# Kernel tuning notes

Hardware: AMD Instinct MI355X
Metric: run time of the kernel (lower is better)

The kernel has to match this reference:

```python
import jax, jax.numpy as jnp
import numpy as np

B, T, I, H, L = 64, 1024, 256, 512, 2

def setup_inputs() -> dict:
    key = jax.random.key(0)
    ks = jax.random.split(key, 1 + 4 * L)
    inp = {"x": jax.random.normal(ks[0], (B, 1, I, T), dtype=jnp.float32)}
    s_in = 1.0 / np.sqrt(H)
    for l in range(L):
        in_dim = I if l == 0 else H
        k0, k1, k2, k3 = ks[1 + 4 * l: 5 + 4 * l]
        inp[f"W_ih{l}"] = jax.random.uniform(k0, (4 * H, in_dim), jnp.float32, -s_in, s_in)
        inp[f"W_hh{l}"] = jax.random.uniform(k1, (4 * H, H), jnp.float32, -s_in, s_in)
        inp[f"b_ih{l}"] = jax.random.uniform(k2, (4 * H,), jnp.float32, -s_in, s_in)
        inp[f"b_hh{l}"] = jax.random.uniform(k3, (4 * H,), jnp.float32, -s_in, s_in)
    return inp

def _lstm_layer(x, W_ih, W_hh, b_ih, b_hh):
    # x: [B, T, in_dim] -> outputs [B, T, H], (h_T, c_T) each [B, H]
    xp = jnp.einsum('bti,gi->btg', x, W_ih) + b_ih + b_hh  # [B, T, 4H]
    h0 = jnp.zeros((x.shape[0], H), x.dtype)
    c0 = jnp.zeros((x.shape[0], H), x.dtype)

    def step(carry, xt):
        h, c = carry
        gates = xt + h @ W_hh.T  # [B, 4H]
        i, f, g, o = jnp.split(gates, 4, axis=-1)  # PyTorch gate order: i,f,g,o
        i = jax.nn.sigmoid(i); f = jax.nn.sigmoid(f)
        g = jnp.tanh(g); o = jax.nn.sigmoid(o)
        c = f * c + i * g
        h = o * jnp.tanh(c)
        return (h, c), h

    (hT, cT), ys = jax.lax.scan(step, (h0, c0), jnp.swapaxes(xp, 0, 1))
    return jnp.swapaxes(ys, 0, 1), hT, cT

def reference(x, W_ih0, W_hh0, b_ih0, b_hh0, W_ih1, W_hh1, b_ih1, b_hh1):
    # x: [B, 1, I, T] -> squeeze(1), permute(0,2,1) -> [B, T, I]
    seq = jnp.transpose(jnp.squeeze(x, 1), (0, 2, 1))
    params = [(W_ih0, W_hh0, b_ih0, b_hh0), (W_ih1, W_hh1, b_ih1, b_hh1)]
    hs, cs = [], []
    out = seq
    for (W_ih, W_hh, b_ih, b_hh) in params:
        out, hT, cT = _lstm_layer(out, W_ih, W_hh, b_ih, b_hh)
        hs.append(hT); cs.append(cT)
    hidden = jnp.stack(hs, 0)  # [L, B, H]
    cell = jnp.stack(cs, 0)    # [L, B, H]
    return (out, (hidden, cell))
```

## Files before the change

kernel.cpp:

```cpp
#include <hip/hip_runtime.h>

#define HB 64
#define HT 1024
#define HI 256
#define HH 512

typedef short short8 __attribute__((ext_vector_type(8)));
typedef float f32x4 __attribute__((ext_vector_type(4)));
typedef int   i32x4 __attribute__((ext_vector_type(4)));

__device__ __forceinline__ unsigned short f2bf(float f) {
    unsigned u = __float_as_uint(f);
    u += 0x7FFF + ((u >> 16) & 1);
    return (unsigned short)(u >> 16);
}
__device__ __forceinline__ float bf2f(unsigned short s) {
    return __uint_as_float(((unsigned)s) << 16);
}
__device__ __forceinline__ float fsigmoid(float x) {
    return __builtin_amdgcn_rcpf(1.0f + __expf(-x));
}
__device__ __forceinline__ float ftanh(float x) {
    return 1.0f - 2.0f * __builtin_amdgcn_rcpf(__expf(2.0f * x) + 1.0f);
}

__device__ __forceinline__ void st_pair16(void* p, i32x4 v) {
    asm volatile("global_store_dwordx4 %0, %1, off sc0 sc1"
                 :: "v"(p), "v"(v) : "memory");
}

__device__ __forceinline__ void lds_fence() {
    asm volatile("s_waitcnt lgkmcnt(0)" ::: "memory");
    __builtin_amdgcn_sched_barrier(0);
}

__device__ __forceinline__ void pull16(const char* base0, int expect, short8* af,
                                       int& fuel) {
    for (;;) {
        i32x4 v[32];
        const char* b = base0;
        #pragma unroll
        for (int bi = 0; bi < 8; ++bi) {
            asm volatile("global_load_dwordx4 %0, %1, off sc0 sc1"
                         : "=v"(v[bi * 4 + 0]) : "v"(b));
            asm volatile("global_load_dwordx4 %0, %1, off offset:16 sc0 sc1"
                         : "=v"(v[bi * 4 + 1]) : "v"(b));
            asm volatile("global_load_dwordx4 %0, %1, off offset:2048 sc0 sc1"
                         : "=v"(v[bi * 4 + 2]) : "v"(b));
            asm volatile("global_load_dwordx4 %0, %1, off offset:2064 sc0 sc1"
                         : "=v"(v[bi * 4 + 3]) : "v"(b));
            b += 4096;
        }
        asm volatile("s_waitcnt vmcnt(0)" ::: "memory");
        __builtin_amdgcn_sched_barrier(0);
        int ok = 1;
        #pragma unroll
        for (int i = 0; i < 32; ++i)
            ok &= (v[i][2] == expect) & (v[i][3] == 0);
        bool done = (__ballot(ok != 0) == ~0ull);
        if (!done) {
            fuel -= 64;
            if (fuel > 0) { __builtin_amdgcn_s_sleep(2); continue; }
        }
        #pragma unroll
        for (int kt = 0; kt < 16; ++kt) {
            union { int i4[4]; short8 s; } u;
            u.i4[0] = v[2 * kt][0];     u.i4[1] = v[2 * kt][1];
            u.i4[2] = v[2 * kt + 1][0]; u.i4[3] = v[2 * kt + 1][1];
            af[kt] = u.s;
        }
        return;
    }
}

__global__ void pack_weights(const float* __restrict__ Wih0, const float* __restrict__ Whh0,
                             const float* __restrict__ bih0, const float* __restrict__ bhh0,
                             const float* __restrict__ Wih1, const float* __restrict__ Whh1,
                             const float* __restrict__ bih1, const float* __restrict__ bhh1,
                             unsigned short* __restrict__ wp0,
                             unsigned short* __restrict__ wp1,
                             float* __restrict__ bs) {
    int idx = blockIdx.x * 256 + threadIdx.x;
    int stride = gridDim.x * 256;
    const int NP0 = 128 * 24 * 512;
    const int NP1 = 128 * 32 * 512;
    for (int e = idx; e < NP0; e += stride) {
        int j = e & 7, l = (e >> 3) & 63, rem = e >> 9;
        int kt = rem % 24, nt = rem / 24;
        int n = nt * 16 + (l & 15);
        int k = kt * 32 + ((l >> 4) << 3) + j;
        float v = (k < HI) ? Wih0[n * HI + k] : Whh0[n * HH + (k - HI)];
        wp0[e] = f2bf(v);
    }
    for (int e = idx; e < NP1; e += stride) {
        int j = e & 7, l = (e >> 3) & 63, rem = e >> 9;
        int kt = rem & 31, nt = rem >> 5;
        int n = nt * 16 + (l & 15);
        int k = kt * 32 + ((l >> 4) << 3) + j;
        float v = (k < HH) ? Wih1[n * HH + k] : Whh1[n * HH + (k - HH)];
        wp1[e] = f2bf(v);
    }
    for (int e = idx; e < 2048; e += stride) {
        bs[e]        = bih0[e] + bhh0[e];
        bs[2048 + e] = bih1[e] + bhh1[e];
    }
}

__global__ void pack_x(const float* __restrict__ x, unsigned short* __restrict__ xp) {
    int tt = blockIdx.x;
    int ii = blockIdx.y;
    int bt = blockIdx.z;
    int w  = threadIdx.x;
    __shared__ unsigned short tile[512][16];
    int tloc = w & 15;
    for (int q = 0; q < 32; ++q) {
        int p = q * 16 + (w >> 4);
        int m = p >> 5, iloc = p & 31;
        int b = bt * 16 + m, i = ii * 32 + iloc, t = tt * 16 + tloc;
        tile[p][tloc] = f2bf(x[((size_t)b * HI + i) * HT + t]);
    }
    __syncthreads();
    int e  = w * 2;
    int l  = e >> 3, j0 = e & 7;
    int m  = l & 15;
    int i0 = ((l >> 4) << 3) + j0;
    for (int ti = 0; ti < 16; ++ti) {
        int t = tt * 16 + ti;
        size_t base = ((size_t)(t * 4 + bt) * 8 + ii) * 512;
        unsigned v0 = tile[m * 32 + i0][ti];
        unsigned v1 = tile[m * 32 + i0 + 1][ti];
        ((unsigned int*)xp)[(base + e) >> 1] = v0 | (v1 << 16);
    }
}

__global__ void init_sync(int* __restrict__ flags,
                          int4* __restrict__ h0r, int4* __restrict__ h1r) {
    int idx = blockIdx.x * 256 + threadIdx.x;
    int stride = gridDim.x * 256;
    for (int e = idx; e < 256; e += stride) flags[e] = 0;
    int4 s; s.x = 0; s.y = 0; s.z = -1; s.w = -1;
    for (int e = idx; e < 32768; e += stride) h0r[e] = s;
    for (int e = idx; e < 16384; e += stride) h1r[e] = s;
}

__global__ void __launch_bounds__(256, 1) lstm_persist(
        const unsigned short* __restrict__ wp0,
        const unsigned short* __restrict__ wp1,
        const float* __restrict__ bs,
        const unsigned short* __restrict__ xp,
        char* __restrict__ h0ring,
        char* __restrict__ h1ring,
        int* __restrict__ flag0,
        int* __restrict__ flag1,
        float* __restrict__ out) {
    __shared__ int4 ldsw[8192];
    __shared__ unsigned short stage_s[1024];

    const int bid   = blockIdx.x;
    const int layer = bid >> 5;
    const int ut    = bid & 31;
    const int tid   = threadIdx.x;
    const int mt    = tid >> 6;
    const int l     = tid & 63;
    const int ul    = l & 15;
    const int q     = l >> 4;
    const int KT    = layer ? 32 : 24;

    const short8* ldsf = (const short8*)ldsw;

    {
        const unsigned short* wsrc = layer ? wp1 : wp0;
        for (int g = 0; g < 4; ++g) {
            const int4* src = (const int4*)(wsrc + (size_t)(g * 32 + ut) * KT * 512);
            int4* dst = ldsw + (size_t)g * KT * 64;
            for (int i = tid; i < KT * 64; i += 256) dst[i] = src[i];
        }
    }
    float bv[4];
    #pragma unroll
    for (int g = 0; g < 4; ++g) bv[g] = bs[layer * 2048 + g * HH + ut * 16 + ul];
    float cc[4] = {0.f, 0.f, 0.f, 0.f};
    __syncthreads();

    const int u = ut * 16 + ul;
    const int stg_w = mt * 256 + (ul >> 3) * 128 + (ul & 7);
    const int ring_sub = (ut >> 1) * 128 + ((2 * ut) & 3) * 32 + l;

    const int* pp0 = (l < 32) ? (flag0 + mt * 32 + l)
                              : (flag1 + mt * 32 + (l - 32));
    const int* pp1 = flag1 + mt * 32 + (l & 31);

    int fuel = 1 << 23;

    for (int t = 0; t < HT; ++t) {
        f32x4 acc[4];
        #pragma unroll
        for (int g = 0; g < 4; ++g) {
            f32x4 a; a[0] = bv[g]; a[1] = bv[g]; a[2] = bv[g]; a[3] = bv[g];
            acc[g] = a;
        }

        if (layer == 0) {
            const bool act  = (l < 32) ? (t > 0) : (t >= 4);
            const int  need = (l < 32) ? t : (t - 3);
            int pf = act ? __hip_atomic_load(pp0, __ATOMIC_RELAXED,
                                             __HIP_MEMORY_SCOPE_AGENT)
                         : 0x7fffffff;

            const short8* xa = (const short8*)xp + ((size_t)t * 4 + mt) * 8 * 64;
            #pragma unroll
            for (int kt = 0; kt < 8; ++kt) {
                short8 a = xa[kt * 64 + l];
                #pragma unroll
                for (int g = 0; g < 4; ++g)
                    acc[g] = __builtin_amdgcn_mfma_f32_16x16x32_bf16(
                        a, ldsf[(g * 24 + kt) * 64 + l], acc[g], 0, 0, 0);
            }
            if (t > 0) {
                for (;;) {
                    if (__ballot(pf >= need) == ~0ull) break;
                    if (--fuel <= 0) break;
                    __builtin_amdgcn_s_sleep(1);
                    if (act) pf = __hip_atomic_load(pp0, __ATOMIC_RELAXED,
                                                    __HIP_MEMORY_SCOPE_AGENT);
                }
                const char* hb = h0ring +
                    (size_t)((((t - 1) & 3) * 4 + mt)) * 32768 + (size_t)l * 32;
                short8 af[16];
                pull16(hb, t - 1, af, fuel);
                #pragma unroll
                for (int kt = 0; kt < 16; ++kt) {
                    #pragma unroll
                    for (int g = 0; g < 4; ++g)
                        acc[g] = __builtin_amdgcn_mfma_f32_16x16x32_bf16(
                            af[kt], ldsf[(g * 24 + 8 + kt) * 64 + l], acc[g], 0, 0, 0);
                }
            }

            #pragma unroll
            for (int r = 0; r < 4; ++r) {
                int m = q * 4 + r;
                int b = mt * 16 + m;
                float iv = fsigmoid(acc[0][r]);
                float fv2 = fsigmoid(acc[1][r]);
                float gv = ftanh(acc[2][r]);
                float ov = fsigmoid(acc[3][r]);
                float c = fv2 * cc[r] + iv * gv;
                cc[r] = c;
                float h = ov * ftanh(c);
                stage_s[stg_w + m * 8] = f2bf(h);
                if (t == HT - 1) {
                    out[33554432 + b * 512 + u] = h;
                    out[33619968 + b * 512 + u] = c;
                }
            }
            lds_fence();

            {
                unsigned s0 = stage_s[tid * 4 + 0], s1 = stage_s[tid * 4 + 1];
                unsigned s2 = stage_s[tid * 4 + 2], s3 = stage_s[tid * 4 + 3];
                i32x4 pv;
                pv[0] = (int)(s0 | (s1 << 16));
                pv[1] = (int)(s2 | (s3 << 16));
                pv[2] = t; pv[3] = 0;
                char* dst = h0ring +
                    ((size_t)((t & 3) * 4 + mt) * 2048 + ring_sub) * 16;
                st_pair16(dst, pv);
            }
            if (l == 0)
                __hip_atomic_store(flag0 + mt * 32 + ut, t + 1,
                                   __ATOMIC_RELAXED, __HIP_MEMORY_SCOPE_AGENT);
            asm volatile("s_waitcnt vmcnt(0)" ::: "memory");
        } else {
            int pf = (t > 0 && l < 32)
                         ? __hip_atomic_load(pp1, __ATOMIC_RELAXED,
                                             __HIP_MEMORY_SCOPE_AGENT)
                         : 0x7fffffff;

            if (t > 0) {
                for (;;) {
                    if (__ballot(pf >= t) == ~0ull) break;
                    if (--fuel <= 0) break;
                    __builtin_amdgcn_s_sleep(1);
                    if (l < 32) pf = __hip_atomic_load(pp1, __ATOMIC_RELAXED,
                                                       __HIP_MEMORY_SCOPE_AGENT);
                }
                const char* hb1 = h1ring +
                    (size_t)((((t - 1) & 1) * 4 + mt)) * 32768 + (size_t)l * 32;
                short8 af1[16];
                pull16(hb1, t - 1, af1, fuel);
                #pragma unroll
                for (int kt = 0; kt < 16; ++kt) {
                    #pragma unroll
                    for (int g = 0; g < 4; ++g)
                        acc[g] = __builtin_amdgcn_mfma_f32_16x16x32_bf16(
                            af1[kt], ldsf[(g * 32 + 16 + kt) * 64 + l], acc[g], 0, 0, 0);
                }
            }
            {
                const char* hb0 = h0ring +
                    (size_t)(((t & 3) * 4 + mt)) * 32768 + (size_t)l * 32;
                short8 af0[16];
                pull16(hb0, t, af0, fuel);
                #pragma unroll
                for (int kt = 0; kt < 16; ++kt) {
                    #pragma unroll
                    for (int g = 0; g < 4; ++g)
                        acc[g] = __builtin_amdgcn_mfma_f32_16x16x32_bf16(
                            af0[kt], ldsf[(g * 32 + kt) * 64 + l], acc[g], 0, 0, 0);
                }
            }

            #pragma unroll
            for (int r = 0; r < 4; ++r) {
                int m = q * 4 + r;
                int b = mt * 16 + m;
                float iv = fsigmoid(acc[0][r]);
                float fv2 = fsigmoid(acc[1][r]);
                float gv = ftanh(acc[2][r]);
                float ov = fsigmoid(acc[3][r]);
                float c = fv2 * cc[r] + iv * gv;
                cc[r] = c;
                float h = ov * ftanh(c);
                stage_s[stg_w + m * 8] = f2bf(h);
                if (t == HT - 1) {
                    out[33554432 + 32768 + b * 512 + u] = h;
                    out[33619968 + 32768 + b * 512 + u] = c;
                }
            }
            lds_fence();

            {
                unsigned s0 = stage_s[tid * 4 + 0], s1 = stage_s[tid * 4 + 1];
                unsigned s2 = stage_s[tid * 4 + 2], s3 = stage_s[tid * 4 + 3];
                i32x4 pv;
                pv[0] = (int)(s0 | (s1 << 16));
                pv[1] = (int)(s2 | (s3 << 16));
                pv[2] = t; pv[3] = 0;
                char* dst = h1ring +
                    ((size_t)((t & 1) * 4 + mt) * 2048 + ring_sub) * 16;
                st_pair16(dst, pv);
            }
            if (l == 0)
                __hip_atomic_store(flag1 + mt * 32 + ut, t + 1,
                                   __ATOMIC_RELAXED, __HIP_MEMORY_SCOPE_AGENT);

            {
                int lb = l >> 2, ch = l & 3;
                int b = mt * 16 + lb;
                const unsigned short* sp = stage_s + mt * 256 + (ch >> 1) * 128 +
                                           lb * 8 + (ch & 1) * 4;
                f32x4 o;
                o[0] = bf2f(sp[0]); o[1] = bf2f(sp[1]);
                o[2] = bf2f(sp[2]); o[3] = bf2f(sp[3]);
                *(f32x4*)&out[((size_t)b * HT + t) * HH + ut * 16 + ch * 4] = o;
            }
            asm volatile("s_waitcnt vmcnt(0)" ::: "memory");
        }
    }
}

extern "C" void kernel_launch(void* const* d_in, const int* in_sizes, int n_in,
                              void* d_out, int out_size, void* d_ws, size_t ws_size,
                              hipStream_t stream) {
    const float* x    = (const float*)d_in[0];
    const float* Wih0 = (const float*)d_in[1];
    const float* Whh0 = (const float*)d_in[2];
    const float* bih0 = (const float*)d_in[3];
    const float* bhh0 = (const float*)d_in[4];
    const float* Wih1 = (const float*)d_in[5];
    const float* Whh1 = (const float*)d_in[6];
    const float* bih1 = (const float*)d_in[7];
    const float* bhh1 = (const float*)d_in[8];

    char* ws = (char*)d_ws;
    unsigned short* wp0 = (unsigned short*)(ws + 0);
    unsigned short* wp1 = (unsigned short*)(ws + 3145728);
    float*          bsv = (float*)(ws + 7340032);
    unsigned short* xp  = (unsigned short*)(ws + 7356416);
    int*   flag0        = (int*)(ws + 40910848);
    int*   flag1        = (int*)(ws + 40911360);
    char*  h0r          = (char*)(ws + 41041920);
    char*  h1r          = (char*)(ws + 41566208);
    float* out = (float*)d_out;

    pack_weights<<<2048, 256, 0, stream>>>(Wih0, Whh0, bih0, bhh0,
                                           Wih1, Whh1, bih1, bhh1, wp0, wp1, bsv);
    pack_x<<<dim3(64, 8, 4), 256, 0, stream>>>(x, xp);
    init_sync<<<64, 256, 0, stream>>>(flag0, (int4*)h0r, (int4*)h1r);

    lstm_persist<<<64, 256, 0, stream>>>(wp0, wp1, bsv, xp, h0r, h1r,
                                         flag0, flag1, out);
}
```

Baseline: 7.487 ms.

## Pin each LSTM layer to one XCD and sync via local L2 instead of MALL

The kernel now launches 256 blocks and uses the XCC_ID register with atomic slot counters so that layer 0 runs on XCD 0 and layer 1 on XCD 1, and surplus blocks exit. Intra-layer hidden-state exchange uses sc0-only stores and loads plus buffer_inv, keeping the polling traffic in the XCD-local L2 rather than going to MALL. Only the layer0-to-layer1 handoff still goes through a MALL ring. Ring buffers are no longer reinitialised on each launch: a generation counter (rb) is bumped every call and embedded in the tags, and explicit flag polling is replaced by tag checks. This relies on the hardware dispatching at least 32 blocks to each of XCDs 0 and 1, and on sc0 coherence semantics holding within one XCD.

```diff
diff --git a/kernel.cpp b/kernel.cpp
--- a/kernel.cpp
+++ b/kernel.cpp
@@ -24,18 +24,65 @@
     return 1.0f - 2.0f * __builtin_amdgcn_rcpf(__expf(2.0f * x) + 1.0f);
 }
 
-__device__ __forceinline__ void st_pair16(void* p, i32x4 v) {
-    asm volatile("global_store_dwordx4 %0, %1, off sc0 sc1"
-                 :: "v"(p), "v"(v) : "memory");
-}
-
+__device__ __forceinline__ void st_pair_loc(void* p, i32x4 v) {
+    asm volatile("global_store_dwordx4 %0, %1, off sc0" :: "v"(p), "v"(v) : "memory");
+}
+__device__ __forceinline__ void st_pair_mall(void* p, i32x4 v) {
+    asm volatile("global_store_dwordx4 %0, %1, off sc0 sc1" :: "v"(p), "v"(v) : "memory");
+}
 __device__ __forceinline__ void lds_fence() {
     asm volatile("s_waitcnt lgkmcnt(0)" ::: "memory");
     __builtin_amdgcn_sched_barrier(0);
 }
-
-__device__ __forceinline__ void pull16(const char* base0, int expect, short8* af,
-                                       int& fuel) {
+__device__ __forceinline__ int ld4m(const int* p) {
+    int v;
+    asm volatile("global_load_dword %0, %1, off sc0 sc1" : "=v"(v) : "v"(p) : "memory");
+    asm volatile("s_waitcnt vmcnt(0)" ::: "memory");
+    __builtin_amdgcn_sched_barrier(0);
+    return v;
+}
+
+__device__ __forceinline__ void pull16_loc(const char* base0, int expect,
+                                           short8* af, int& fuel) {
+    for (;;) {
+        asm volatile("buffer_inv" ::: "memory");
+        i32x4 v[32];
+        const char* b = base0;
+        #pragma unroll
+        for (int bi = 0; bi < 8; ++bi) {
+            asm volatile("global_load_dwordx4 %0, %1, off sc0"
+                         : "=v"(v[bi * 4 + 0]) : "v"(b));
+            asm volatile("global_load_dwordx4 %0, %1, off offset:16 sc0"
+                         : "=v"(v[bi * 4 + 1]) : "v"(b));
+            asm volatile("global_load_dwordx4 %0, %1, off offset:2048 sc0"
+                         : "=v"(v[bi * 4 + 2]) : "v"(b));
+            asm volatile("global_load_dwordx4 %0, %1, off offset:2064 sc0"
+                         : "=v"(v[bi * 4 + 3]) : "v"(b));
+            b += 4096;
+        }
+        asm volatile("s_waitcnt vmcnt(0)" ::: "memory");
+        __builtin_amdgcn_sched_barrier(0);
+        int ok = 1;
+        #pragma unroll
+        for (int i = 0; i < 32; ++i)
+            ok &= (v[i][2] == expect) & (v[i][3] == 0);
+        bool done = (__ballot(ok != 0) == ~0ull);
+        if (!done) {
+            fuel -= 64;
+            if (fuel > 0) { __builtin_amdgcn_s_sleep(2); continue; }
+        }
+        #pragma unroll
+        for (int kt = 0; kt < 16; ++kt) {
+            union { int i4[4]; short8 s; } u;
+            u.i4[0] = v[2 * kt][0];     u.i4[1] = v[2 * kt][1];
+            u.i4[2] = v[2 * kt + 1][0]; u.i4[3] = v[2 * kt + 1][1];
+            af[kt] = u.s;
+        }
+        return;
+    }
+}
+__device__ __forceinline__ void pull16_mall(const char* base0, int expect,
+                                            short8* af, int& fuel) {
     for (;;) {
         i32x4 v[32];
         const char* b = base0;
@@ -133,14 +180,10 @@
     }
 }
 
-__global__ void init_sync(int* __restrict__ flags,
-                          int4* __restrict__ h0r, int4* __restrict__ h1r) {
-    int idx = blockIdx.x * 256 + threadIdx.x;
-    int stride = gridDim.x * 256;
-    for (int e = idx; e < 256; e += stride) flags[e] = 0;
-    int4 s; s.x = 0; s.y = 0; s.z = -1; s.w = -1;
-    for (int e = idx; e < 32768; e += stride) h0r[e] = s;
-    for (int e = idx; e < 16384; e += stride) h1r[e] = s;
+__global__ void init_sync(int* __restrict__ s) {
+    int i = threadIdx.x;
+    if (i == 0) { s[0] = 0; s[1] = 0; s[2] += 2048; }
+    if (i >= 64 && i < 192) s[i] = 0;
 }
 
 __global__ void __launch_bounds__(256, 1) lstm_persist(
@@ -148,24 +191,43 @@
         const unsigned short* __restrict__ wp1,
         const float* __restrict__ bs,
         const unsigned short* __restrict__ xp,
-        char* __restrict__ h0ring,
-        char* __restrict__ h1ring,
-        int* __restrict__ flag0,
-        int* __restrict__ flag1,
+        char* __restrict__ h0loc,
+        char* __restrict__ h1loc,
+        char* __restrict__ h0mall,
+        int* __restrict__ sync,
         float* __restrict__ out) {
     __shared__ int4 ldsw[8192];
     __shared__ unsigned short stage_s[1024];
-
-    const int bid   = blockIdx.x;
-    const int layer = bid >> 5;
-    const int ut    = bid & 31;
-    const int tid   = threadIdx.x;
-    const int mt    = tid >> 6;
-    const int l     = tid & 63;
-    const int ul    = l & 15;
-    const int q     = l >> 4;
-    const int KT    = layer ? 32 : 24;
-
+    __shared__ int rs[2];
+
+    int* f1m = sync + 64;
+    const int tid = threadIdx.x;
+    int xcd;
+    asm volatile("s_getreg_b32 %0, hwreg(HW_REG_XCC_ID)" : "=s"(xcd));
+    if (tid == 0) {
+        int role = -1, slot = 0;
+        if (xcd == 0) {
+            slot = __hip_atomic_fetch_add(sync + 0, 1, __ATOMIC_RELAXED,
+                                          __HIP_MEMORY_SCOPE_AGENT);
+            if (slot < 32) role = 0;
+        } else if (xcd == 1) {
+            slot = __hip_atomic_fetch_add(sync + 1, 1, __ATOMIC_RELAXED,
+                                          __HIP_MEMORY_SCOPE_AGENT);
+            if (slot < 32) role = 1;
+        }
+        rs[0] = role; rs[1] = slot;
+    }
+    __syncthreads();
+    const int layer = rs[0];
+    const int ut    = rs[1];
+    if (layer < 0) return;
+
+    const int rb = sync[2];
+    const int mt = tid >> 6;
+    const int l  = tid & 63;
+    const int ul = l & 15;
+    const int q  = l >> 4;
+    const int KT = layer ? 32 : 24;
     const short8* ldsf = (const short8*)ldsw;
 
     {
@@ -185,27 +247,20 @@
     const int u = ut * 16 + ul;
     const int stg_w = mt * 256 + (ul >> 3) * 128 + (ul & 7);
     const int ring_sub = (ut >> 1) * 128 + ((2 * ut) & 3) * 32 + l;
-
-    const int* pp0 = (l < 32) ? (flag0 + mt * 32 + l)
-                              : (flag1 + mt * 32 + (l - 32));
-    const int* pp1 = flag1 + mt * 32 + (l & 31);
-
-    int fuel = 1 << 23;
-
-    for (int t = 0; t < HT; ++t) {
-        f32x4 acc[4];
-        #pragma unroll
-        for (int g = 0; g < 4; ++g) {
-            f32x4 a; a[0] = bv[g]; a[1] = bv[g]; a[2] = bv[g]; a[3] = bv[g];
-            acc[g] = a;
-        }
-
-        if (layer == 0) {
-            const bool act  = (l < 32) ? (t > 0) : (t >= 4);
-            const int  need = (l < 32) ? t : (t - 3);
-            int pf = act ? __hip_atomic_load(pp0, __ATOMIC_RELAXED,
-                                             __HIP_MEMORY_SCOPE_AGENT)
-                         : 0x7fffffff;
+    int fuel = 1 << 22;
+
+    if (layer == 0) {
+        for (int t = 0; t < HT; ++t) {
+            f32x4 acc[4];
+            #pragma unroll
+            for (int g = 0; g < 4; ++g) {
+                f32x4 a; a[0] = bv[g]; a[1] = bv[g]; a[2] = bv[g]; a[3] = bv[g];
+                acc[g] = a;
+            }
+            int adv = 0x7fffffff;
+            if (t >= 4 && l < 32)
+                asm volatile("global_load_dword %0, %1, off sc0 sc1"
+                             : "=v"(adv) : "v"(f1m + mt * 32 + l) : "memory");
 
             const short8* xa = (const short8*)xp + ((size_t)t * 4 + mt) * 8 * 64;
             #pragma unroll
@@ -217,17 +272,9 @@
                         a, ldsf[(g * 24 + kt) * 64 + l], acc[g], 0, 0, 0);
             }
             if (t > 0) {
-                for (;;) {
-                    if (__ballot(pf >= need) == ~0ull) break;
-                    if (--fuel <= 0) break;
-                    __builtin_amdgcn_s_sleep(1);
-                    if (act) pf = __hip_atomic_load(pp0, __ATOMIC_RELAXED,
-                                                    __HIP_MEMORY_SCOPE_AGENT);
-                }
-                const char* hb = h0ring +
-                    (size_t)((((t - 1) & 3) * 4 + mt)) * 32768 + (size_t)l * 32;
                 short8 af[16];
-                pull16(hb, t - 1, af, fuel);
+                pull16_loc(h0loc + (size_t)(((t - 1) & 1) * 4 + mt) * 32768 +
+                           (size_t)l * 32, rb + t - 1, af, fuel);
                 #pragma unroll
                 for (int kt = 0; kt < 16; ++kt) {
                     #pragma unroll
@@ -236,7 +283,6 @@
                             af[kt], ldsf[(g * 24 + 8 + kt) * 64 + l], acc[g], 0, 0, 0);
                 }
             }
-
             #pragma unroll
             for (int r = 0; r < 4; ++r) {
                 int m = q * 4 + r;
@@ -255,40 +301,60 @@
                 }
             }
             lds_fence();
-
+            unsigned s0 = stage_s[tid * 4 + 0], s1 = stage_s[tid * 4 + 1];
+            unsigned s2 = stage_s[tid * 4 + 2], s3 = stage_s[tid * 4 + 3];
+            i32x4 pv;
+            pv[0] = (int)(s0 | (s1 << 16));
+            pv[1] = (int)(s2 | (s3 << 16));
+            pv[2] = rb + t; pv[3] = 0;
+
+            if (t >= 4) {
+                __builtin_amdgcn_sched_barrier(0);
+                if (__ballot(adv >= t - 3) != ~0ull) {
+                    const int* ap = f1m + mt * 32 + (l & 31);
+                    for (;;) {
+                        int v2 = (l < 32) ? ld4m(ap) : 0x7fffffff;
+                        if (__ballot(v2 >= t - 3) == ~0ull) break;
+                        if (--fuel <= 0) break;
+                        __builtin_amdgcn_s_sleep(1);
+                    }
+                }
+            }
+            st_pair_loc(h0loc + ((size_t)((t & 1) * 4 + mt) * 2048 + ring_sub) * 16, pv);
+            st_pair_mall(h0mall + ((size_t)((t & 3) * 4 + mt) * 2048 + ring_sub) * 16, pv);
+        }
+    } else {
+        for (int t = 0; t < HT; ++t) {
+            f32x4 acc[4];
+            #pragma unroll
+            for (int g = 0; g < 4; ++g) {
+                f32x4 a; a[0] = bv[g]; a[1] = bv[g]; a[2] = bv[g]; a[3] = bv[g];
+                acc[g] = a;
+            }
+            short8 af1[16];
+            if (t > 0)
+                pull16_loc(h1loc + (size_t)(((t - 1) & 1) * 4 + mt) * 32768 +
+                           (size_t)l * 32, rb + t - 1, af1, fuel);
+
+            i32x4 vm[32];
+            const char* mbase = h0mall + (size_t)((t & 3) * 4 + mt) * 32768 +
+                                (size_t)l * 32;
             {
-                unsigned s0 = stage_s[tid * 4 + 0], s1 = stage_s[tid * 4 + 1];
-                unsigned s2 = stage_s[tid * 4 + 2], s3 = stage_s[tid * 4 + 3];
-                i32x4 pv;
-                pv[0] = (int)(s0 | (s1 << 16));
-                pv[1] = (int)(s2 | (s3 << 16));
-                pv[2] = t; pv[3] = 0;
-                char* dst = h0ring +
-                    ((size_t)((t & 3) * 4 + mt) * 2048 + ring_sub) * 16;
-                st_pair16(dst, pv);
-            }
-            if (l == 0)
-                __hip_atomic_store(flag0 + mt * 32 + ut, t + 1,
-                                   __ATOMIC_RELAXED, __HIP_MEMORY_SCOPE_AGENT);
-            asm volatile("s_waitcnt vmcnt(0)" ::: "memory");
-        } else {
-            int pf = (t > 0 && l < 32)
-                         ? __hip_atomic_load(pp1, __ATOMIC_RELAXED,
-                                             __HIP_MEMORY_SCOPE_AGENT)
-                         : 0x7fffffff;
-
+                const char* b = mbase;
+                #pragma unroll
+                for (int bi = 0; bi < 8; ++bi) {
+                    asm volatile("global_load_dwordx4 %0, %1, off sc0 sc1"
+                                 : "=v"(vm[bi * 4 + 0]) : "v"(b));
+                    asm volatile("global_load_dwordx4 %0, %1, off offset:16 sc0 sc1"
+                                 : "=v"(vm[bi * 4 + 1]) : "v"(b));
+                    asm volatile("global_load_dwordx4 %0, %1, off offset:2048 sc0 sc1"
+                                 : "=v"(vm[bi * 4 + 2]) : "v"(b));
+                    asm volatile("global_load_dwordx4 %0, %1, off offset:2064 sc0 sc1"
+                                 : "=v"(vm[bi * 4 + 3]) : "v"(b));
+                    b += 4096;
+                }
+            }
             if (t > 0) {
-                for (;;) {
-                    if (__ballot(pf >= t) == ~0ull) break;
-                    if (--fuel <= 0) break;
-                    __builtin_amdgcn_s_sleep(1);
-                    if (l < 32) pf = __hip_atomic_load(pp1, __ATOMIC_RELAXED,
-                                                       __HIP_MEMORY_SCOPE_AGENT);
-                }
-                const char* hb1 = h1ring +
-                    (size_t)((((t - 1) & 1) * 4 + mt)) * 32768 + (size_t)l * 32;
-                short8 af1[16];
-                pull16(hb1, t - 1, af1, fuel);
                 #pragma unroll
                 for (int kt = 0; kt < 16; ++kt) {
                     #pragma unroll
@@ -297,20 +363,33 @@
                             af1[kt], ldsf[(g * 32 + 16 + kt) * 64 + l], acc[g], 0, 0, 0);
                 }
             }
+            asm volatile("s_waitcnt vmcnt(0)" ::: "memory");
+            __builtin_amdgcn_sched_barrier(0);
+            short8 af0[16];
             {
-                const char* hb0 = h0ring +
-                    (size_t)(((t & 3) * 4 + mt)) * 32768 + (size_t)l * 32;
-                short8 af0[16];
-                pull16(hb0, t, af0, fuel);
-                #pragma unroll
-                for (int kt = 0; kt < 16; ++kt) {
+                int ok = 1;
+                #pragma unroll
+                for (int i = 0; i < 32; ++i)
+                    ok &= (vm[i][2] == rb + t) & (vm[i][3] == 0);
+                if (__ballot(ok != 0) == ~0ull) {
                     #pragma unroll
-                    for (int g = 0; g < 4; ++g)
-                        acc[g] = __builtin_amdgcn_mfma_f32_16x16x32_bf16(
-                            af0[kt], ldsf[(g * 32 + kt) * 64 + l], acc[g], 0, 0, 0);
-                }
-            }
-
+                    for (int kt = 0; kt < 16; ++kt) {
+                        union { int i4[4]; short8 s; } uu;
+                        uu.i4[0] = vm[2 * kt][0];     uu.i4[1] = vm[2 * kt][1];
+                        uu.i4[2] = vm[2 * kt + 1][0]; uu.i4[3] = vm[2 * kt + 1][1];
+                        af0[kt] = uu.s;
+                    }
+                } else {
+                    pull16_mall(mbase, rb + t, af0, fuel);
+                }
+            }
+            #pragma unroll
+            for (int kt = 0; kt < 16; ++kt) {
+                #pragma unroll
+                for (int g = 0; g < 4; ++g)
+                    acc[g] = __builtin_amdgcn_mfma_f32_16x16x32_bf16(
+                        af0[kt], ldsf[(g * 32 + kt) * 64 + l], acc[g], 0, 0, 0);
+            }
             #pragma unroll
             for (int r = 0; r < 4; ++r) {
                 int m = q * 4 + r;
@@ -329,22 +408,16 @@
                 }
             }
             lds_fence();
-
-            {
-                unsigned s0 = stage_s[tid * 4 + 0], s1 = stage_s[tid * 4 + 1];
-                unsigned s2 = stage_s[tid * 4 + 2], s3 = stage_s[tid * 4 + 3];
-                i32x4 pv;
-                pv[0] = (int)(s0 | (s1 << 16));
-                pv[1] = (int)(s2 | (s3 << 16));
-                pv[2] = t; pv[3] = 0;
-                char* dst = h1ring +
-                    ((size_t)((t & 1) * 4 + mt) * 2048 + ring_sub) * 16;
-                st_pair16(dst, pv);
-            }
+            unsigned s0 = stage_s[tid * 4 + 0], s1 = stage_s[tid * 4 + 1];
+            unsigned s2 = stage_s[tid * 4 + 2], s3 = stage_s[tid * 4 + 3];
+            i32x4 pv;
+            pv[0] = (int)(s0 | (s1 << 16));
+            pv[1] = (int)(s2 | (s3 << 16));
+            pv[2] = rb + t; pv[3] = 0;
+            st_pair_loc(h1loc + ((size_t)((t & 1) * 4 + mt) * 2048 + ring_sub) * 16, pv);
             if (l == 0)
-                __hip_atomic_store(flag1 + mt * 32 + ut, t + 1,
+                __hip_atomic_store(f1m + mt * 32 + ut, t + 1,
                                    __ATOMIC_RELAXED, __HIP_MEMORY_SCOPE_AGENT);
-
             {
                 int lb = l >> 2, ch = l & 3;
                 int b = mt * 16 + lb;
@@ -355,7 +428,6 @@
                 o[2] = bf2f(sp[2]); o[3] = bf2f(sp[3]);
                 *(f32x4*)&out[((size_t)b * HT + t) * HH + ut * 16 + ch * 4] = o;
             }
-            asm volatile("s_waitcnt vmcnt(0)" ::: "memory");
         }
     }
 }
@@ -378,17 +450,17 @@
     unsigned short* wp1 = (unsigned short*)(ws + 3145728);
     float*          bsv = (float*)(ws + 7340032);
     unsigned short* xp  = (unsigned short*)(ws + 7356416);
-    int*   flag0        = (int*)(ws + 40910848);
-    int*   flag1        = (int*)(ws + 40911360);
-    char*  h0r          = (char*)(ws + 41041920);
-    char*  h1r          = (char*)(ws + 41566208);
+    int*   sync         = (int*)(ws + 40910848);
+    char*  h0loc        = ws + 40911872;
+    char*  h1loc        = ws + 41174016;
+    char*  h0mall       = ws + 41436160;
     float* out = (float*)d_out;
 
     pack_weights<<<2048, 256, 0, stream>>>(Wih0, Whh0, bih0, bhh0,
                                            Wih1, Whh1, bih1, bhh1, wp0, wp1, bsv);
     pack_x<<<dim3(64, 8, 4), 256, 0, stream>>>(x, xp);
-    init_sync<<<64, 256, 0, stream>>>(flag0, (int4*)h0r, (int4*)h1r);
-
-    lstm_persist<<<64, 256, 0, stream>>>(wp0, wp1, bsv, xp, h0r, h1r,
-                                         flag0, flag1, out);
-}
+    init_sync<<<1, 256, 0, stream>>>(sync);
+
+    lstm_persist<<<256, 256, 0, stream>>>(wp0, wp1, bsv, xp,
+                                          h0loc, h1loc, h0mall, sync, out);
+}
```

Measured after the change: 16.98 ms. +126.8%, slower.
